# Optimization experiments

Measured on AMD Instinct MI355X. Metric: run time of the kernel, lower is better.

## Reference

```python
import jax, jax.numpy as jnp
import numpy as np

N_NODES = 50000
N_EDGES = 600000
N_PATHS = 3
IN_DIM = 128
OUT_DIM = 128  # out_size(16) * heads(8)
SEM_HID = 128


def setup_inputs() -> dict:
    key = jax.random.key(0)
    ks = jax.random.split(key, 8)
    h = jax.random.normal(ks[0], (N_NODES, IN_DIM), jnp.float32)
    edge_src = jax.random.randint(ks[1], (N_PATHS, N_EDGES), 0, N_NODES, dtype=jnp.int32)
    edge_dst = jax.random.randint(ks[2], (N_PATHS, N_EDGES), 0, N_NODES, dtype=jnp.int32)
    W_gc = jax.random.normal(ks[3], (N_PATHS, IN_DIM, OUT_DIM), jnp.float32) * (1.0 / np.sqrt(IN_DIM))
    b_gc = jnp.zeros((N_PATHS, OUT_DIM), jnp.float32)
    w1 = jax.random.normal(ks[4], (OUT_DIM, SEM_HID), jnp.float32) * (1.0 / np.sqrt(OUT_DIM))
    b1 = jnp.zeros((SEM_HID,), jnp.float32)
    w2 = jax.random.normal(ks[5], (SEM_HID, 1), jnp.float32) * (1.0 / np.sqrt(SEM_HID))
    return {"h": h, "W_gc": W_gc, "b_gc": b_gc, "w1": w1, "b1": b1, "w2": w2,
            "edge_src": edge_src, "edge_dst": edge_dst}


def reference(h, W_gc, b_gc, w1, b1, w2, edge_src, edge_dst):
    n = h.shape[0]

    def graph_conv(W, b, src, dst):
        # DGL GraphConv, norm='both': D_out^{-1/2} message -> sum -> D_in^{-1/2}, + bias
        ones = jnp.ones(src.shape, h.dtype)
        deg_out = jax.ops.segment_sum(ones, src, num_segments=n)
        deg_in = jax.ops.segment_sum(ones, dst, num_segments=n)
        x = h * jax.lax.rsqrt(jnp.maximum(deg_out, 1.0))[:, None]
        x = x @ W  # [N, OUT_DIM]
        agg = jax.ops.segment_sum(x[src], dst, num_segments=n)
        return agg * jax.lax.rsqrt(jnp.maximum(deg_in, 1.0))[:, None] + b

    # z: [N, P, D] stacked per-metapath embeddings
    z = jax.vmap(graph_conv, in_axes=(0, 0, 0, 0), out_axes=1)(W_gc, b_gc, edge_src, edge_dst)
    # semantic attention: mean over nodes of per-(node,path) scores
    w = jnp.mean(jnp.tanh(z @ w1 + b1) @ w2, axis=0)  # [P, 1]
    beta = jax.nn.softmax(w, axis=0)                   # [P, 1]
    return jnp.sum(beta * z, axis=1)                   # [N, D]
```

## Files before the change

### kernel.cpp

```cpp
#include <hip/hip_runtime.h>
#include <math.h>

#define N_NODES 50000
#define N_EDGES 600000
#define N_PATHS 3
#define DIM 128
#define NROWS_ALL (N_PATHS * N_NODES)
#define NE_ALL (N_PATHS * N_EDGES)
#define SCAN_BLOCKS ((NROWS_ALL + 1023) / 1024)
#define NTILES_ALL (NROWS_ALL / 16)
#define NTILES_N (N_NODES / 16)

#define HB_BINS 16384
#define HB_RANGES 4
#define HB_CHUNKS 12
#define CHUNK_E (N_EDGES / HB_CHUNKS)

typedef __attribute__((ext_vector_type(8))) short bf16x8;
typedef __attribute__((ext_vector_type(4))) float f32x4;

__device__ __forceinline__ unsigned short f2bf(float f) {
    unsigned u = __float_as_uint(f);
    u += 0x7FFF + ((u >> 16) & 1);
    return (unsigned short)(u >> 16);
}
__device__ __forceinline__ float tanh_fast(float x) {
    return 1.0f - 2.0f / (__expf(2.0f * x) + 1.0f);
}

__global__ void conv_h(const float* __restrict__ h, unsigned int* __restrict__ hb) {
    int i = blockIdx.x * blockDim.x + threadIdx.x;
    if (i >= N_NODES * DIM / 8) return;
    const float4* h4 = (const float4*)h;
    float4 a = h4[2 * i], b = h4[2 * i + 1];
    uint4 o;
    o.x = f2bf(a.x) | ((unsigned)f2bf(a.y) << 16);
    o.y = f2bf(a.z) | ((unsigned)f2bf(a.w) << 16);
    o.z = f2bf(b.x) | ((unsigned)f2bf(b.y) << 16);
    o.w = f2bf(b.z) | ((unsigned)f2bf(b.w) << 16);
    ((uint4*)hb)[i] = o;
}

__global__ void conv_w(const float* __restrict__ W_gc, const float* __restrict__ w1,
                       uint4* __restrict__ wsw) {
    int i = blockIdx.x * blockDim.x + threadIdx.x;
    if (i >= (N_PATHS + 1) * 2048) return;
    int mat = i >> 11;
    int rem = i & 2047;
    int frag = rem >> 6, lane = rem & 63;
    int n0 = frag >> 2, q = frag & 3;
    int quad = lane >> 4, m = lane & 15;
    int n = n0 * 16 + m;
    int kbase = q * 32 + quad * 8;
    const float* src = (mat < N_PATHS) ? (W_gc + (size_t)mat * DIM * DIM) : w1;
    unsigned short t[8];
#pragma unroll
    for (int j = 0; j < 8; ++j) t[j] = f2bf(src[(size_t)(kbase + j) * DIM + n]);
    uint4 o;
    o.x = t[0] | ((unsigned)t[1] << 16);
    o.y = t[2] | ((unsigned)t[3] << 16);
    o.z = t[4] | ((unsigned)t[5] << 16);
    o.w = t[6] | ((unsigned)t[7] << 16);
    wsw[i] = o;
}

__global__ __launch_bounds__(256) void hist_kernel(const int* __restrict__ esrc,
                                                   const int* __restrict__ edst,
                                                   int* __restrict__ pcnt_out,
                                                   int* __restrict__ pcnt_in) {
    __shared__ int bins[HB_BINS];
    int tid = threadIdx.x;
    {   int4* b4 = (int4*)bins;
        for (int i = tid; i < HB_BINS / 4; i += 256) b4[i] = make_int4(0, 0, 0, 0);
    }
    int b = blockIdx.x;
    int c = b % HB_CHUNKS;
    int r = (b / HB_CHUNKS) % HB_RANGES;
    int p = (b / (HB_CHUNKS * HB_RANGES)) % N_PATHS;
    int type = b / (HB_CHUNKS * HB_RANGES * N_PATHS);
    const int* ptr = (type == 0 ? esrc : edst) + (size_t)p * N_EDGES + c * CHUNK_E;
    int r0 = r * HB_BINS;
    __syncthreads();
    const int4* p4 = (const int4*)ptr;
    for (int i = tid; i < CHUNK_E / 4; i += 256) {
        int4 v = p4[i];
        int l0 = v.x - r0; if ((unsigned)l0 < HB_BINS) atomicAdd(&bins[l0], 1);
        int l1 = v.y - r0; if ((unsigned)l1 < HB_BINS) atomicAdd(&bins[l1], 1);
        int l2 = v.z - r0; if ((unsigned)l2 < HB_BINS) atomicAdd(&bins[l2], 1);
        int l3 = v.w - r0; if ((unsigned)l3 < HB_BINS) atomicAdd(&bins[l3], 1);
    }
    __syncthreads();
    int bound = min(HB_BINS, N_NODES - r0);
    int* dst = (type == 0 ? pcnt_out : pcnt_in) + (size_t)c * NROWS_ALL + p * N_NODES + r0;
    const int4* b4 = (const int4*)bins;
    int4* d4 = (int4*)dst;
    for (int i = tid; i < bound / 4; i += 256) d4[i] = b4[i];
}

__global__ void merge_kernel(const int* __restrict__ pcnt_out, const int* __restrict__ pcnt_in,
                             int* __restrict__ cnt_out, int* __restrict__ cnt_in,
                             float* __restrict__ sc_out) {
    int pn = blockIdx.x * blockDim.x + threadIdx.x;
    if (pn < NROWS_ALL) {
        int si = 0, so = 0;
#pragma unroll
        for (int c = 0; c < HB_CHUNKS; ++c) {
            si += pcnt_in [(size_t)c * NROWS_ALL + pn];
            so += pcnt_out[(size_t)c * NROWS_ALL + pn];
        }
        cnt_in[pn] = si;
        cnt_out[pn] = so;
        sc_out[pn] = rsqrtf(fmaxf((float)so, 1.0f));
    }
}

__global__ __launch_bounds__(256) void scan_pass1(const int* __restrict__ cnt,
                                                  int* __restrict__ partial) {
    __shared__ int lds[256];
    int t = threadIdx.x;
    int base = blockIdx.x * 1024 + t * 4;
    int4 v = make_int4(0, 0, 0, 0);
    if (base < NROWS_ALL) v = *(const int4*)(cnt + base);
    int s = v.x + v.y + v.z + v.w;
    lds[t] = s; __syncthreads();
    for (int off = 1; off < 256; off <<= 1) {
        int u = (t >= off) ? lds[t - off] : 0;
        __syncthreads();
        lds[t] += u;
        __syncthreads();
    }
    if (t == 255) partial[blockIdx.x] = lds[255];
}

__global__ __launch_bounds__(256) void scan_pass2(int* __restrict__ partial) {
    __shared__ int lds[256];
    int t = threadIdx.x;
    int s = (t < SCAN_BLOCKS) ? partial[t] : 0;
    lds[t] = s; __syncthreads();
    for (int off = 1; off < 256; off <<= 1) {
        int u = (t >= off) ? lds[t - off] : 0;
        __syncthreads();
        lds[t] += u;
        __syncthreads();
    }
    if (t < SCAN_BLOCKS) partial[t] = lds[t] - s;
}

__global__ __launch_bounds__(256) void scan_pass3(const int* __restrict__ cnt,
                                                  const int* __restrict__ partial,
                                                  int* __restrict__ cursor) {
    __shared__ int lds[256];
    int t = threadIdx.x;
    int base = blockIdx.x * 1024 + t * 4;
    int4 v = make_int4(0, 0, 0, 0);
    if (base < NROWS_ALL) v = *(const int4*)(cnt + base);
    int s = v.x + v.y + v.z + v.w;
    lds[t] = s; __syncthreads();
    for (int off = 1; off < 256; off <<= 1) {
        int u = (t >= off) ? lds[t - off] : 0;
        __syncthreads();
        lds[t] += u;
        __syncthreads();
    }
    if (base < NROWS_ALL) {
        int run = partial[blockIdx.x] + lds[t] - s;
        int vv[4] = {v.x, v.y, v.z, v.w};
#pragma unroll
        for (int j = 0; j < 4; ++j) { cursor[base + j] = run; run += vv[j]; }
    }
}

__global__ void chunkbase_kernel(const int* __restrict__ cursor, int* __restrict__ pcnt_in) {
    int pn = blockIdx.x * blockDim.x + threadIdx.x;
    if (pn < NROWS_ALL) {
        int base = cursor[pn];
#pragma unroll
        for (int c = 0; c < HB_CHUNKS; ++c) {
            int t = pcnt_in[(size_t)c * NROWS_ALL + pn];
            pcnt_in[(size_t)c * NROWS_ALL + pn] = base;
            base += t;
        }
    }
}

__global__ __launch_bounds__(256) void fill2_kernel(const int* __restrict__ esrc,
                                                    const int* __restrict__ edst,
                                                    const int* __restrict__ pcnt_in,
                                                    unsigned short* __restrict__ col) {
    __shared__ int curs[HB_BINS];
    int tid = threadIdx.x;
    int b = blockIdx.x;
    int c = b % HB_CHUNKS;
    int r = (b / HB_CHUNKS) % HB_RANGES;
    int p = b / (HB_CHUNKS * HB_RANGES);
    int r0 = r * HB_BINS;
    int bound = min(HB_BINS, N_NODES - r0);
    const int* basep = pcnt_in + (size_t)c * NROWS_ALL + p * N_NODES + r0;
    for (int i = tid; i < bound; i += 256) curs[i] = basep[i];
    __syncthreads();
    const int4* sp4 = (const int4*)(esrc + (size_t)p * N_EDGES + c * CHUNK_E);
    const int4* dp4 = (const int4*)(edst + (size_t)p * N_EDGES + c * CHUNK_E);
    for (int i = tid; i < CHUNK_E / 4; i += 256) {
        int4 dv = dp4[i];
        int4 sv = sp4[i];
        int l0 = dv.x - r0; if ((unsigned)l0 < HB_BINS) { int pos = atomicAdd(&curs[l0], 1); col[pos] = (unsigned short)sv.x; }
        int l1 = dv.y - r0; if ((unsigned)l1 < HB_BINS) { int pos = atomicAdd(&curs[l1], 1); col[pos] = (unsigned short)sv.y; }
        int l2 = dv.z - r0; if ((unsigned)l2 < HB_BINS) { int pos = atomicAdd(&curs[l2], 1); col[pos] = (unsigned short)sv.z; }
        int l3 = dv.w - r0; if ((unsigned)l3 < HB_BINS) { int pos = atomicAdd(&curs[l3], 1); col[pos] = (unsigned short)sv.w; }
    }
}

__global__ __launch_bounds__(256) void gather_kernel(const int* __restrict__ cursor,
                                                     const int* __restrict__ cnt_in,
                                                     const unsigned short* __restrict__ col,
                                                     const float* __restrict__ sc_out,
                                                     const uint4* __restrict__ hb4,
                                                     uint4* __restrict__ aggb4) {
    int wid = blockIdx.x * 4 + (threadIdx.x >> 6);
    int lane = threadIdx.x & 63;
    int ss = lane >> 4;
    int ln = lane & 15;
    if (wid >= NROWS_ALL) return;
    int p = wid / N_NODES;
    int beg = cursor[wid];
    int end = beg + cnt_in[wid];
    const float* scp = sc_out + p * N_NODES;
    float acc[8] = {};
    for (int e = beg + ss; e < end; e += 4) {
        int s = col[e];
        float sc = scp[s];
        uint4 v = hb4[s * 16 + ln];
        acc[0] = fmaf(__uint_as_float(v.x << 16),        sc, acc[0]);
        acc[1] = fmaf(__uint_as_float(v.x & 0xFFFF0000u), sc, acc[1]);
        acc[2] = fmaf(__uint_as_float(v.y << 16),        sc, acc[2]);
        acc[3] = fmaf(__uint_as_float(v.y & 0xFFFF0000u), sc, acc[3]);
        acc[4] = fmaf(__uint_as_float(v.z << 16),        sc, acc[4]);
        acc[5] = fmaf(__uint_as_float(v.z & 0xFFFF0000u), sc, acc[5]);
        acc[6] = fmaf(__uint_as_float(v.w << 16),        sc, acc[6]);
        acc[7] = fmaf(__uint_as_float(v.w & 0xFFFF0000u), sc, acc[7]);
    }
#pragma unroll
    for (int j = 0; j < 8; ++j) {
        acc[j] += __shfl_xor(acc[j], 16, 64);
        acc[j] += __shfl_xor(acc[j], 32, 64);
    }
    if (ss == 0) {
        uint4 o;
        o.x = f2bf(acc[0]) | ((unsigned)f2bf(acc[1]) << 16);
        o.y = f2bf(acc[2]) | ((unsigned)f2bf(acc[3]) << 16);
        o.z = f2bf(acc[4]) | ((unsigned)f2bf(acc[5]) << 16);
        o.w = f2bf(acc[6]) | ((unsigned)f2bf(acc[7]) << 16);
        int t = wid >> 4, m = wid & 15, q = ln >> 2, qd = ln & 3;
        aggb4[(size_t)t * 256 + q * 64 + qd * 16 + m] = o;
    }
}

__global__ __launch_bounds__(256, 4) void score_pass(const uint4* __restrict__ aggb4,
                                                     const uint4* __restrict__ wsw,
                                                     const int* __restrict__ cnt_in,
                                                     const float* __restrict__ b_gc,
                                                     const float* __restrict__ b1,
                                                     const float* __restrict__ w2,
                                                     float* __restrict__ scorep) {
    __shared__ float zS[4][16][132];
    int wave = threadIdx.x >> 6, lane = threadIdx.x & 63;
    int m = lane & 15, quad = lane >> 4;
    int t = blockIdx.x * 4 + wave;
    if (t >= NTILES_ALL) return;
    int r0 = t * 16;
    int p = r0 / N_NODES;
    const uint4* At = aggb4 + (size_t)t * 256 + lane;
    bf16x8 a[4];
#pragma unroll
    for (int q = 0; q < 4; ++q) a[q] = *(const bf16x8*)&At[q * 64];
    float s[4];
#pragma unroll
    for (int rg = 0; rg < 4; ++rg)
        s[rg] = rsqrtf(fmaxf((float)cnt_in[r0 + quad * 4 + rg], 1.0f));
    const uint4* Bp = wsw + (size_t)p * 2048 + lane;
    const float* bgc = b_gc + p * DIM;
    float (*zw)[132] = zS[wave];
#pragma unroll
    for (int n0 = 0; n0 < 8; ++n0) {
        f32x4 acc = {0.f, 0.f, 0.f, 0.f};
#pragma unroll
        for (int q = 0; q < 4; ++q) {
            bf16x8 b = *(const bf16x8*)&Bp[(n0 * 4 + q) * 64];
            acc = __builtin_amdgcn_mfma_f32_16x16x32_bf16(a[q], b, acc, 0, 0, 0);
        }
        int colj = n0 * 16 + m;
        float bias = bgc[colj];
#pragma unroll
        for (int rg = 0; rg < 4; ++rg)
            zw[quad * 4 + rg][colj] = acc[rg] * s[rg] + bias;
    }
    bf16x8 sa[4];
#pragma unroll
    for (int q = 0; q < 4; ++q) {
        const float* pr = &zw[m][q * 32 + quad * 8];
        float4 f0 = *(const float4*)pr;
        float4 f1 = *(const float4*)(pr + 4);
        bf16x8 tt;
        tt[0] = f2bf(f0.x); tt[1] = f2bf(f0.y); tt[2] = f2bf(f0.z); tt[3] = f2bf(f0.w);
        tt[4] = f2bf(f1.x); tt[5] = f2bf(f1.y); tt[6] = f2bf(f1.z); tt[7] = f2bf(f1.w);
        sa[q] = tt;
    }
    const uint4* W1 = wsw + (size_t)N_PATHS * 2048 + lane;
    float rsum[4] = {0.f, 0.f, 0.f, 0.f};
#pragma unroll
    for (int n0 = 0; n0 < 8; ++n0) {
        f32x4 acc = {0.f, 0.f, 0.f, 0.f};
#pragma unroll
        for (int q = 0; q < 4; ++q) {
            bf16x8 b = *(const bf16x8*)&W1[(n0 * 4 + q) * 64];
            acc = __builtin_amdgcn_mfma_f32_16x16x32_bf16(sa[q], b, acc, 0, 0, 0);
        }
        int colj = n0 * 16 + m;
        float bj = b1[colj], wj = w2[colj];
#pragma unroll
        for (int rg = 0; rg < 4; ++rg)
            rsum[rg] += tanh_fast(acc[rg] + bj) * wj;
    }
#pragma unroll
    for (int off = 1; off < 64; off <<= 1)
#pragma unroll
        for (int rg = 0; rg < 4; ++rg) rsum[rg] += __shfl_xor(rsum[rg], off, 64);
    if (lane == 0)
        scorep[t] = rsum[0] + rsum[1] + rsum[2] + rsum[3];
}

__global__ __launch_bounds__(1024) void beta_kernel(const float* __restrict__ scorep,
                                                    float* __restrict__ beta) {
    __shared__ float red[3][1024];
    int t = threadIdx.x;
    float a0 = 0.f, a1 = 0.f, a2 = 0.f;
    for (int i = t; i < NTILES_ALL; i += 1024) {
        float v = scorep[i];
        int p = (i * 16) / N_NODES;
        if (p == 0) a0 += v; else if (p == 1) a1 += v; else a2 += v;
    }
    red[0][t] = a0; red[1][t] = a1; red[2][t] = a2;
    __syncthreads();
    for (int off = 512; off > 0; off >>= 1) {
        if (t < off) {
            red[0][t] += red[0][t + off];
            red[1][t] += red[1][t + off];
            red[2][t] += red[2][t + off];
        }
        __syncthreads();
    }
    if (t == 0) {
        float a = red[0][0] / (float)N_NODES;
        float b = red[1][0] / (float)N_NODES;
        float c = red[2][0] / (float)N_NODES;
        float mx = fmaxf(a, fmaxf(b, c));
        float e0 = expf(a - mx), e1 = expf(b - mx), e2 = expf(c - mx);
        float sm = e0 + e1 + e2;
        beta[0] = e0 / sm; beta[1] = e1 / sm; beta[2] = e2 / sm;
    }
}

__global__ __launch_bounds__(256, 4) void out_pass(const uint4* __restrict__ aggb4,
                                                   const uint4* __restrict__ wsw,
                                                   const int* __restrict__ cnt_in,
                                                   const float* __restrict__ b_gc,
                                                   const float* __restrict__ beta,
                                                   float* __restrict__ out) {
    __shared__ float zS[4][16][132];
    int wave = threadIdx.x >> 6, lane = threadIdx.x & 63;
    int m = lane & 15, quad = lane >> 4;
    int t = blockIdx.x * 4 + wave;
    if (t >= NTILES_N) return;
    int r0 = t * 16;
    float of[8][4] = {};
#pragma unroll
    for (int p = 0; p < N_PATHS; ++p) {
        const uint4* At = aggb4 + (size_t)(p * NTILES_N + t) * 256 + lane;
        bf16x8 a[4];
#pragma unroll
        for (int q = 0; q < 4; ++q) a[q] = *(const bf16x8*)&At[q * 64];
        float s[4];
#pragma unroll
        for (int rg = 0; rg < 4; ++rg)
            s[rg] = rsqrtf(fmaxf((float)cnt_in[p * N_NODES + r0 + quad * 4 + rg], 1.0f));
        float bp = beta[p];
        const uint4* Bp = wsw + (size_t)p * 2048 + lane;
        const float* bgc = b_gc + p * DIM;
#pragma unroll
        for (int n0 = 0; n0 < 8; ++n0) {
            f32x4 acc = {0.f, 0.f, 0.f, 0.f};
#pragma unroll
            for (int q = 0; q < 4; ++q) {
                bf16x8 b = *(const bf16x8*)&Bp[(n0 * 4 + q) * 64];
                acc = __builtin_amdgcn_mfma_f32_16x16x32_bf16(a[q], b, acc, 0, 0, 0);
            }
            float bias = bgc[n0 * 16 + m];
#pragma unroll
            for (int rg = 0; rg < 4; ++rg)
                of[n0][rg] = fmaf(bp, acc[rg] * s[rg] + bias, of[n0][rg]);
        }
    }
    float (*zw)[132] = zS[wave];
#pragma unroll
    for (int n0 = 0; n0 < 8; ++n0)
#pragma unroll
        for (int rg = 0; rg < 4; ++rg)
            zw[quad * 4 + rg][n0 * 16 + m] = of[n0][rg];
#pragma unroll
    for (int i = 0; i < 8; ++i) {
        int fi = i * 64 + lane;
        int row = fi >> 5, c4 = fi & 31;
        float4 v = *(const float4*)&zw[row][c4 * 4];
        *(float4*)(out + (size_t)(r0 + row) * DIM + c4 * 4) = v;
    }
}

extern "C" void kernel_launch(void* const* d_in, const int* in_sizes, int n_in,
                              void* d_out, int out_size, void* d_ws, size_t ws_size,
                              hipStream_t stream) {
    const float* h    = (const float*)d_in[0];
    const float* W_gc = (const float*)d_in[1];
    const float* b_gc = (const float*)d_in[2];
    const float* w1   = (const float*)d_in[3];
    const float* b1   = (const float*)d_in[4];
    const float* w2   = (const float*)d_in[5];
    const int* esrc   = (const int*)d_in[6];
    const int* edst   = (const int*)d_in[7];
    float* out        = (float*)d_out;

    int*   cnt_out = (int*)d_ws;
    int*   cnt_in  = cnt_out + NROWS_ALL;
    float* beta    = (float*)d_ws + 300004;
    int*   partial = (int*)d_ws + 300032;
    float* sc_out  = (float*)d_ws + 300288;
    float* scorep  = (float*)d_ws + 300288;
    uint4* wsw     = (uint4*)((int*)d_ws + 450288);
    unsigned int* aggb = (unsigned int*)((int*)d_ws + 483056);
    int*   cursor  = (int*)d_ws + 10083056;
    unsigned short* col = (unsigned short*)((int*)d_ws + 10233056);
    unsigned int*   hb  = (unsigned int*)((int*)d_ws + 11133056);
    int*   pcnt_out = (int*)d_ws + 14333056;
    int*   pcnt_in  = (int*)d_ws + 16133056;

    conv_h<<<(N_NODES * DIM / 8 + 255) / 256, 256, 0, stream>>>(h, hb);
    conv_w<<<((N_PATHS + 1) * 2048 + 255) / 256, 256, 0, stream>>>(W_gc, w1, wsw);

    hist_kernel<<<2 * N_PATHS * HB_RANGES * HB_CHUNKS, 256, 0, stream>>>(
        esrc, edst, pcnt_out, pcnt_in);

    merge_kernel<<<(NROWS_ALL + 255) / 256, 256, 0, stream>>>(
        pcnt_out, pcnt_in, cnt_out, cnt_in, sc_out);

    scan_pass1<<<SCAN_BLOCKS, 256, 0, stream>>>(cnt_in, partial);
    scan_pass2<<<1, 256, 0, stream>>>(partial);
    scan_pass3<<<SCAN_BLOCKS, 256, 0, stream>>>(cnt_in, partial, cursor);

    chunkbase_kernel<<<(NROWS_ALL + 255) / 256, 256, 0, stream>>>(cursor, pcnt_in);

    fill2_kernel<<<N_PATHS * HB_RANGES * HB_CHUNKS, 256, 0, stream>>>(
        esrc, edst, pcnt_in, col);

    gather_kernel<<<(NROWS_ALL + 3) / 4, 256, 0, stream>>>(
        cursor, cnt_in, col, sc_out, (const uint4*)hb, (uint4*)aggb);

    score_pass<<<(NTILES_ALL + 3) / 4, 256, 0, stream>>>(
        (const uint4*)aggb, wsw, cnt_in, b_gc, b1, w2, scorep);

    beta_kernel<<<1, 1024, 0, stream>>>(scorep, beta);

    out_pass<<<(NTILES_N + 3) / 4, 256, 0, stream>>>(
        (const uint4*)aggb, wsw, cnt_in, b_gc, beta, out);
}
```

Baseline: 322.6 us.

## Fuse merge/chunkbase into scan passes, double histogram chunks, unroll gather loops

Folds the per-chunk count merge and degree scale into the first scan pass, and the per-chunk base computation into the third scan pass, removing two kernel launches and using vectorized int4 accesses. Doubles the number of histogram chunks for more block-level parallelism in the histogram and fill kernels, and unrolls their edge loops by two. Unrolls the gather loop by two to overlap more independent loads. More chunks increases partial-count buffer size and the merge traffic per node, and requires more workspace.

Result: faster. 280.7 us (-13.0%).

```diff
diff --git a/kernel.cpp b/kernel.cpp
--- a/kernel.cpp
+++ b/kernel.cpp
@@ -13,7 +13,7 @@
 
 #define HB_BINS 16384
 #define HB_RANGES 4
-#define HB_CHUNKS 12
+#define HB_CHUNKS 24
 #define CHUNK_E (N_EDGES / HB_CHUNKS)
 
 typedef __attribute__((ext_vector_type(8))) short bf16x8;
@@ -82,12 +82,17 @@
     int r0 = r * HB_BINS;
     __syncthreads();
     const int4* p4 = (const int4*)ptr;
-    for (int i = tid; i < CHUNK_E / 4; i += 256) {
-        int4 v = p4[i];
-        int l0 = v.x - r0; if ((unsigned)l0 < HB_BINS) atomicAdd(&bins[l0], 1);
-        int l1 = v.y - r0; if ((unsigned)l1 < HB_BINS) atomicAdd(&bins[l1], 1);
-        int l2 = v.z - r0; if ((unsigned)l2 < HB_BINS) atomicAdd(&bins[l2], 1);
-        int l3 = v.w - r0; if ((unsigned)l3 < HB_BINS) atomicAdd(&bins[l3], 1);
+    for (int i = tid * 2; i < CHUNK_E / 4; i += 512) {
+        int4 a = p4[i];
+        int4 bb = p4[i + 1];
+        int l0 = a.x - r0;  if ((unsigned)l0 < HB_BINS) atomicAdd(&bins[l0], 1);
+        int l1 = a.y - r0;  if ((unsigned)l1 < HB_BINS) atomicAdd(&bins[l1], 1);
+        int l2 = a.z - r0;  if ((unsigned)l2 < HB_BINS) atomicAdd(&bins[l2], 1);
+        int l3 = a.w - r0;  if ((unsigned)l3 < HB_BINS) atomicAdd(&bins[l3], 1);
+        int l4 = bb.x - r0; if ((unsigned)l4 < HB_BINS) atomicAdd(&bins[l4], 1);
+        int l5 = bb.y - r0; if ((unsigned)l5 < HB_BINS) atomicAdd(&bins[l5], 1);
+        int l6 = bb.z - r0; if ((unsigned)l6 < HB_BINS) atomicAdd(&bins[l6], 1);
+        int l7 = bb.w - r0; if ((unsigned)l7 < HB_BINS) atomicAdd(&bins[l7], 1);
     }
     __syncthreads();
     int bound = min(HB_BINS, N_NODES - r0);
@@ -97,25 +102,63 @@
     for (int i = tid; i < bound / 4; i += 256) d4[i] = b4[i];
 }
 
-__global__ void merge_kernel(const int* __restrict__ pcnt_out, const int* __restrict__ pcnt_in,
-                             int* __restrict__ cnt_out, int* __restrict__ cnt_in,
-                             float* __restrict__ sc_out) {
-    int pn = blockIdx.x * blockDim.x + threadIdx.x;
-    if (pn < NROWS_ALL) {
-        int si = 0, so = 0;
+__global__ __launch_bounds__(256) void scan_pass1(const int* __restrict__ pcnt_out,
+                                                  const int* __restrict__ pcnt_in,
+                                                  int* __restrict__ cnt_out,
+                                                  int* __restrict__ cnt_in,
+                                                  float* __restrict__ sc_out,
+                                                  int* __restrict__ partial) {
+    __shared__ int lds[256];
+    int t = threadIdx.x;
+    int base = blockIdx.x * 1024 + t * 4;
+    int4 ci = make_int4(0, 0, 0, 0);
+    if (base < NROWS_ALL) {
+        int4 co = make_int4(0, 0, 0, 0);
 #pragma unroll
         for (int c = 0; c < HB_CHUNKS; ++c) {
-            si += pcnt_in [(size_t)c * NROWS_ALL + pn];
-            so += pcnt_out[(size_t)c * NROWS_ALL + pn];
+            int4 vi = *(const int4*)(pcnt_in + (size_t)c * NROWS_ALL + base);
+            int4 vo = *(const int4*)(pcnt_out + (size_t)c * NROWS_ALL + base);
+            ci.x += vi.x; ci.y += vi.y; ci.z += vi.z; ci.w += vi.w;
+            co.x += vo.x; co.y += vo.y; co.z += vo.z; co.w += vo.w;
         }
-        cnt_in[pn] = si;
-        cnt_out[pn] = so;
-        sc_out[pn] = rsqrtf(fmaxf((float)so, 1.0f));
-    }
-}
-
-__global__ __launch_bounds__(256) void scan_pass1(const int* __restrict__ cnt,
-                                                  int* __restrict__ partial) {
+        *(int4*)(cnt_in + base) = ci;
+        *(int4*)(cnt_out + base) = co;
+        float4 sc;
+        sc.x = rsqrtf(fmaxf((float)co.x, 1.0f));
+        sc.y = rsqrtf(fmaxf((float)co.y, 1.0f));
+        sc.z = rsqrtf(fmaxf((float)co.z, 1.0f));
+        sc.w = rsqrtf(fmaxf((float)co.w, 1.0f));
+        *(float4*)(sc_out + base) = sc;
+    }
+    int s = ci.x + ci.y + ci.z + ci.w;
+    lds[t] = s; __syncthreads();
+    for (int off = 1; off < 256; off <<= 1) {
+        int u = (t >= off) ? lds[t - off] : 0;
+        __syncthreads();
+        lds[t] += u;
+        __syncthreads();
+    }
+    if (t == 255) partial[blockIdx.x] = lds[255];
+}
+
+__global__ __launch_bounds__(256) void scan_pass2(int* __restrict__ partial) {
+    __shared__ int lds[256];
+    int t = threadIdx.x;
+    int s = (t < SCAN_BLOCKS) ? partial[t] : 0;
+    lds[t] = s; __syncthreads();
+    for (int off = 1; off < 256; off <<= 1) {
+        int u = (t >= off) ? lds[t - off] : 0;
+        __syncthreads();
+        lds[t] += u;
+        __syncthreads();
+    }
+    if (t < SCAN_BLOCKS) partial[t] = lds[t] - s;
+}
+
+__global__ __launch_bounds__(256) void scan_pass3(const int* __restrict__ cnt,
+                                                  const int* __restrict__ partial,
+                                                  int* __restrict__ cursor,
+                                                  int* __restrict__ pcnt_in) {
     __shared__ int lds[256];
     int t = threadIdx.x;
     int base = blockIdx.x * 1024 + t * 4;
@@ -129,56 +172,17 @@
         lds[t] += u;
         __syncthreads();
     }
-    if (t == 255) partial[blockIdx.x] = lds[255];
-}
-
-__global__ __launch_bounds__(256) void scan_pass2(int* __restrict__ partial) {
-    __shared__ int lds[256];
-    int t = threadIdx.x;
-    int s = (t < SCAN_BLOCKS) ? partial[t] : 0;
-    lds[t] = s; __syncthreads();
-    for (int off = 1; off < 256; off <<= 1) {
-        int u = (t >= off) ? lds[t - off] : 0;
-        __syncthreads();
-        lds[t] += u;
-        __syncthreads();
-    }
-    if (t < SCAN_BLOCKS) partial[t] = lds[t] - s;
-}
-
-__global__ __launch_bounds__(256) void scan_pass3(const int* __restrict__ cnt,
-                                                  const int* __restrict__ partial,
-                                                  int* __restrict__ cursor) {
-    __shared__ int lds[256];
-    int t = threadIdx.x;
-    int base = blockIdx.x * 1024 + t * 4;
-    int4 v = make_int4(0, 0, 0, 0);
-    if (base < NROWS_ALL) v = *(const int4*)(cnt + base);
-    int s = v.x + v.y + v.z + v.w;
-    lds[t] = s; __syncthreads();
-    for (int off = 1; off < 256; off <<= 1) {
-        int u = (t >= off) ? lds[t - off] : 0;
-        __syncthreads();
-        lds[t] += u;
-        __syncthreads();
-    }
     if (base < NROWS_ALL) {
         int run = partial[blockIdx.x] + lds[t] - s;
         int vv[4] = {v.x, v.y, v.z, v.w};
-#pragma unroll
-        for (int j = 0; j < 4; ++j) { cursor[base + j] = run; run += vv[j]; }
-    }
-}
-
-__global__ void chunkbase_kernel(const int* __restrict__ cursor, int* __restrict__ pcnt_in) {
-    int pn = blockIdx.x * blockDim.x + threadIdx.x;
-    if (pn < NROWS_ALL) {
-        int base = cursor[pn];
+        int rb[4];
+#pragma unroll
+        for (int j = 0; j < 4; ++j) { cursor[base + j] = run; rb[j] = run; run += vv[j]; }
 #pragma unroll
         for (int c = 0; c < HB_CHUNKS; ++c) {
-            int t = pcnt_in[(size_t)c * NROWS_ALL + pn];
-            pcnt_in[(size_t)c * NROWS_ALL + pn] = base;
-            base += t;
+            int4 pc = *(const int4*)(pcnt_in + (size_t)c * NROWS_ALL + base);
+            *(int4*)(pcnt_in + (size_t)c * NROWS_ALL + base) = make_int4(rb[0], rb[1], rb[2], rb[3]);
+            rb[0] += pc.x; rb[1] += pc.y; rb[2] += pc.z; rb[3] += pc.w;
         }
     }
 }
@@ -200,13 +204,19 @@
     __syncthreads();
     const int4* sp4 = (const int4*)(esrc + (size_t)p * N_EDGES + c * CHUNK_E);
     const int4* dp4 = (const int4*)(edst + (size_t)p * N_EDGES + c * CHUNK_E);
-    for (int i = tid; i < CHUNK_E / 4; i += 256) {
-        int4 dv = dp4[i];
-        int4 sv = sp4[i];
-        int l0 = dv.x - r0; if ((unsigned)l0 < HB_BINS) { int pos = atomicAdd(&curs[l0], 1); col[pos] = (unsigned short)sv.x; }
-        int l1 = dv.y - r0; if ((unsigned)l1 < HB_BINS) { int pos = atomicAdd(&curs[l1], 1); col[pos] = (unsigned short)sv.y; }
-        int l2 = dv.z - r0; if ((unsigned)l2 < HB_BINS) { int pos = atomicAdd(&curs[l2], 1); col[pos] = (unsigned short)sv.z; }
-        int l3 = dv.w - r0; if ((unsigned)l3 < HB_BINS) { int pos = atomicAdd(&curs[l3], 1); col[pos] = (unsigned short)sv.w; }
+    for (int i = tid * 2; i < CHUNK_E / 4; i += 512) {
+        int4 dv0 = dp4[i];
+        int4 dv1 = dp4[i + 1];
+        int4 sv0 = sp4[i];
+        int4 sv1 = sp4[i + 1];
+        int l0 = dv0.x - r0; if ((unsigned)l0 < HB_BINS) { int pos = atomicAdd(&curs[l0], 1); col[pos] = (unsigned short)sv0.x; }
+        int l1 = dv0.y - r0; if ((unsigned)l1 < HB_BINS) { int pos = atomicAdd(&curs[l1], 1); col[pos] = (unsigned short)sv0.y; }
+        int l2 = dv0.z - r0; if ((unsigned)l2 < HB_BINS) { int pos = atomicAdd(&curs[l2], 1); col[pos] = (unsigned short)sv0.z; }
+        int l3 = dv0.w - r0; if ((unsigned)l3 < HB_BINS) { int pos = atomicAdd(&curs[l3], 1); col[pos] = (unsigned short)sv0.w; }
+        int l4 = dv1.x - r0; if ((unsigned)l4 < HB_BINS) { int pos = atomicAdd(&curs[l4], 1); col[pos] = (unsigned short)sv1.x; }
+        int l5 = dv1.y - r0; if ((unsigned)l5 < HB_BINS) { int pos = atomicAdd(&curs[l5], 1); col[pos] = (unsigned short)sv1.y; }
+        int l6 = dv1.z - r0; if ((unsigned)l6 < HB_BINS) { int pos = atomicAdd(&curs[l6], 1); col[pos] = (unsigned short)sv1.z; }
+        int l7 = dv1.w - r0; if ((unsigned)l7 < HB_BINS) { int pos = atomicAdd(&curs[l7], 1); col[pos] = (unsigned short)sv1.w; }
     }
 }
 
@@ -226,18 +236,43 @@
     int end = beg + cnt_in[wid];
     const float* scp = sc_out + p * N_NODES;
     float acc[8] = {};
-    for (int e = beg + ss; e < end; e += 4) {
-        int s = col[e];
-        float sc = scp[s];
-        uint4 v = hb4[s * 16 + ln];
-        acc[0] = fmaf(__uint_as_float(v.x << 16),        sc, acc[0]);
-        acc[1] = fmaf(__uint_as_float(v.x & 0xFFFF0000u), sc, acc[1]);
-        acc[2] = fmaf(__uint_as_float(v.y << 16),        sc, acc[2]);
-        acc[3] = fmaf(__uint_as_float(v.y & 0xFFFF0000u), sc, acc[3]);
-        acc[4] = fmaf(__uint_as_float(v.z << 16),        sc, acc[4]);
-        acc[5] = fmaf(__uint_as_float(v.z & 0xFFFF0000u), sc, acc[5]);
-        acc[6] = fmaf(__uint_as_float(v.w << 16),        sc, acc[6]);
-        acc[7] = fmaf(__uint_as_float(v.w & 0xFFFF0000u), sc, acc[7]);
+    int e = beg + ss;
+    for (; e + 4 < end; e += 8) {
+        int s0 = col[e];
+        int s1 = col[e + 4];
+        float c0 = scp[s0];
+        float c1 = scp[s1];
+        uint4 v0 = hb4[s0 * 16 + ln];
+        uint4 v1 = hb4[s1 * 16 + ln];
+        acc[0] = fmaf(__uint_as_float(v0.x << 16),        c0, acc[0]);
+        acc[1] = fmaf(__uint_as_float(v0.x & 0xFFFF0000u), c0, acc[1]);
+        acc[2] = fmaf(__uint_as_float(v0.y << 16),        c0, acc[2]);
+        acc[3] = fmaf(__uint_as_float(v0.y & 0xFFFF0000u), c0, acc[3]);
+        acc[4] = fmaf(__uint_as_float(v0.z << 16),        c0, acc[4]);
+        acc[5] = fmaf(__uint_as_float(v0.z & 0xFFFF0000u), c0, acc[5]);
+        acc[6] = fmaf(__uint_as_float(v0.w << 16),        c0, acc[6]);
+        acc[7] = fmaf(__uint_as_float(v0.w & 0xFFFF0000u), c0, acc[7]);
+        acc[0] = fmaf(__uint_as_float(v1.x << 16),        c1, acc[0]);
+        acc[1] = fmaf(__uint_as_float(v1.x & 0xFFFF0000u), c1, acc[1]);
+        acc[2] = fmaf(__uint_as_float(v1.y << 16),        c1, acc[2]);
+        acc[3] = fmaf(__uint_as_float(v1.y & 0xFFFF0000u), c1, acc[3]);
+        acc[4] = fmaf(__uint_as_float(v1.z << 16),        c1, acc[4]);
+        acc[5] = fmaf(__uint_as_float(v1.z & 0xFFFF0000u), c1, acc[5]);
+        acc[6] = fmaf(__uint_as_float(v1.w << 16),        c1, acc[6]);
+        acc[7] = fmaf(__uint_as_float(v1.w & 0xFFFF0000u), c1, acc[7]);
+    }
+    if (e < end) {
+        int s0 = col[e];
+        float c0 = scp[s0];
+        uint4 v0 = hb4[s0 * 16 + ln];
+        acc[0] = fmaf(__uint_as_float(v0.x << 16),        c0, acc[0]);
+        acc[1] = fmaf(__uint_as_float(v0.x & 0xFFFF0000u), c0, acc[1]);
+        acc[2] = fmaf(__uint_as_float(v0.y << 16),        c0, acc[2]);
+        acc[3] = fmaf(__uint_as_float(v0.y & 0xFFFF0000u), c0, acc[3]);
+        acc[4] = fmaf(__uint_as_float(v0.z << 16),        c0, acc[4]);
+        acc[5] = fmaf(__uint_as_float(v0.z & 0xFFFF0000u), c0, acc[5]);
+        acc[6] = fmaf(__uint_as_float(v0.w << 16),        c0, acc[6]);
+        acc[7] = fmaf(__uint_as_float(v0.w & 0xFFFF0000u), c0, acc[7]);
     }
 #pragma unroll
     for (int j = 0; j < 8; ++j) {
@@ -440,7 +475,7 @@
     unsigned short* col = (unsigned short*)((int*)d_ws + 10233056);
     unsigned int*   hb  = (unsigned int*)((int*)d_ws + 11133056);
     int*   pcnt_out = (int*)d_ws + 14333056;
-    int*   pcnt_in  = (int*)d_ws + 16133056;
+    int*   pcnt_in  = (int*)d_ws + 17933056;
 
     conv_h<<<(N_NODES * DIM / 8 + 255) / 256, 256, 0, stream>>>(h, hb);
     conv_w<<<((N_PATHS + 1) * 2048 + 255) / 256, 256, 0, stream>>>(W_gc, w1, wsw);
@@ -448,14 +483,10 @@
     hist_kernel<<<2 * N_PATHS * HB_RANGES * HB_CHUNKS, 256, 0, stream>>>(
         esrc, edst, pcnt_out, pcnt_in);
 
-    merge_kernel<<<(NROWS_ALL + 255) / 256, 256, 0, stream>>>(
-        pcnt_out, pcnt_in, cnt_out, cnt_in, sc_out);
-
-    scan_pass1<<<SCAN_BLOCKS, 256, 0, stream>>>(cnt_in, partial);
+    scan_pass1<<<SCAN_BLOCKS, 256, 0, stream>>>(
+        pcnt_out, pcnt_in, cnt_out, cnt_in, sc_out, partial);
     scan_pass2<<<1, 256, 0, stream>>>(partial);
-    scan_pass3<<<SCAN_BLOCKS, 256, 0, stream>>>(cnt_in, partial, cursor);
-
-    chunkbase_kernel<<<(NROWS_ALL + 255) / 256, 256, 0, stream>>>(cursor, pcnt_in);
+    scan_pass3<<<SCAN_BLOCKS, 256, 0, stream>>>(cnt_in, partial, cursor, pcnt_in);
 
     fill2_kernel<<<N_PATHS * HB_RANGES * HB_CHUNKS, 256, 0, stream>>>(
         esrc, edst, pcnt_in, col);
```
